# Kernel tuning notes

Hardware: AMD Instinct MI355X
Metric: run time of the kernel (lower is better)

Reference implementation:

```python
import jax, jax.numpy as jnp
import numpy as np

GAZE_DIR = -1.0  # dataset != 'eyediap'
B, V, VM, LAT = 64, 5023, 3500, 556
D_IN = 3 * 224 * 224


def _skew(v):  # [B,3] -> [B,3,3]
    z = jnp.zeros_like(v[:, 0])
    return jnp.stack([
        jnp.stack([z, -v[:, 2], v[:, 1]], axis=1),
        jnp.stack([v[:, 2], z, -v[:, 0]], axis=1),
        jnp.stack([-v[:, 1], v[:, 0], z], axis=1)], axis=1)


def _axis_angle_to_matrix(aa):  # [B,3] -> [B,3,3], Rodrigues
    theta = jnp.linalg.norm(aa, axis=1, keepdims=True)
    axis = aa / jnp.maximum(theta, 1e-8)
    K = _skew(axis)
    s = jnp.sin(theta)[:, :, None]
    c = jnp.cos(theta)[:, :, None]
    return jnp.eye(3, dtype=aa.dtype) + s * K + (1.0 - c) * (K @ K)


def _find_gaze_R(init_gaze):  # rotation taking init_gaze -> [0,0,GAZE_DIR]
    a = init_gaze[:, 0, :]
    a = a / jnp.linalg.norm(a, axis=1, keepdims=True)
    b = jnp.broadcast_to(jnp.array([0.0, 0.0, GAZE_DIR], a.dtype), a.shape)
    v = jnp.cross(a, b)
    c = jnp.sum(a * b, axis=1)
    K = _skew(v)
    return jnp.eye(3, dtype=a.dtype) + K + (K @ K) * (1.0 / (1.0 + c + 1e-8))[:, None, None]


def _apply_eyeball_rotation(eyeball, centre, rot2):
    aa = jnp.concatenate([rot2, jnp.zeros_like(rot2[:, :1])], axis=1)
    R = _axis_angle_to_matrix(aa)
    return jnp.einsum('bvl,bli->bvi', eyeball - centre, R) + centre


def _forward(x, enc_W, enc_b, v_template, shape_basis, camera_parameters,
             landmarks, masked_landmarks, face_mask, lmask, rmask):
    b = x.shape[0]
    latent = x.reshape(b, -1) @ enc_W + enc_b  # encoder stub
    shape_p = latent[:, :400]
    face_rot = latent[:, 545:548]
    face_t = latent[:, 548:551]
    face_scale = latent[:, 551:552] + 1.0
    l_rot = latent[:, 552:554]
    r_rot = latent[:, 554:556]

    # FLAME shape model stub: template + linear blendshapes
    vert = v_template[None] + jnp.einsum('bs,svc->bvc', shape_p, shape_basis)
    vmean = vert.mean(axis=1, keepdims=True)
    vert = (jnp.einsum('bvl,bli->bvi', vert - vmean, _axis_angle_to_matrix(face_rot))
            * face_scale[:, :, None] + face_t[:, None, :])

    l_eye = vert[:, lmask]
    r_eye = vert[:, rmask]
    l_c = l_eye.mean(axis=1, keepdims=True)
    r_c = r_eye.mean(axis=1, keepdims=True)
    idx4 = landmarks[jnp.array([19, 22, 25, 28])]
    idx2 = landmarks[jnp.array([14, 18])]
    face_centre = (vert[:, idx4].mean(1) + vert[:, idx2].mean(1)) / 2.0

    l_init = vert[:, None, 4051] - l_c
    l_init = l_init / jnp.linalg.norm(l_init, axis=2, keepdims=True)
    r_init = vert[:, None, 4597] - r_c
    r_init = r_init / jnp.linalg.norm(r_init, axis=2, keepdims=True)

    le = jnp.einsum('bvl,bli->bvi', l_eye - l_c, _find_gaze_R(l_init)) + l_c
    re = jnp.einsum('bvl,bli->bvi', r_eye - r_c, _find_gaze_R(r_init)) + r_c
    le = _apply_eyeball_rotation(le, l_c, l_rot)
    re = _apply_eyeball_rotation(re, r_c, r_rot)
    # masks are disjoint: vert_no_eyes + vert_eyes == scatter back rotated eyes
    vert = vert.at[:, lmask].set(le).at[:, rmask].set(re)

    gdir = jnp.broadcast_to(jnp.array([0.0, 0.0, GAZE_DIR], vert.dtype), (b, 1, 3))
    zc = jnp.zeros((b, 1, 3), vert.dtype)
    left_gaze = _apply_eyeball_rotation(gdir, zc, l_rot)
    right_gaze = _apply_eyeball_rotation(gdir, zc, r_rot)

    lr_cross = jnp.cross(right_gaze, left_gaze, axis=2)
    A = jnp.concatenate([left_gaze, -right_gaze, lr_cross], axis=1).transpose(0, 2, 1)
    rhs = (r_c - l_c).transpose(0, 2, 1)
    sol = jnp.linalg.solve(A, rhs)  # [B,3,1]
    gp_l = l_c + sol[:, 0:1, :] * left_gaze
    gp_r = r_c + sol[:, 1:2, :] * right_gaze
    gp_mid = (gp_l + gp_r) / 2.0
    dist = jnp.linalg.norm(gp_l - gp_r, axis=2)  # [B,1]

    vmk = vert[:, face_mask]
    fl3d = vmk[:, masked_landmarks]
    # renderer stub: pinhole projection with [B,3,4] camera
    homog = jnp.concatenate([vmk, jnp.ones_like(vmk[..., :1])], axis=-1)
    p = jnp.einsum('bij,bvj->bvi', camera_parameters, homog)
    z = p[..., 2:3]
    zs = jnp.where(z >= 0, 1.0, -1.0) * jnp.maximum(jnp.abs(z), 1e-3)
    vert_img = jnp.concatenate([p[..., :2] / zs, z], axis=-1)

    dist_row = jnp.repeat(dist[:, :, None], 3, axis=2)  # [B,1,3]
    out = jnp.concatenate([
        vmk, vert_img, fl3d, l_c, r_c, face_centre[:, None, :],
        gp_l, gp_r, gp_mid,
        l_c + left_gaze * 1000.0, r_c + right_gaze * 1000.0,
        left_gaze, right_gaze, dist_row], axis=1)  # [B, 2*VM+68+11, 3]
    return out


def setup_inputs() -> dict:
    key = jax.random.key(0)
    ks = jax.random.split(key, 8)
    x = jax.random.normal(ks[0], (B, 3, 224, 224), jnp.float32)
    enc_W = jax.random.normal(ks[1], (D_IN, LAT), jnp.float32) * 1e-3
    enc_b = jax.random.normal(ks[2], (LAT,), jnp.float32) * 0.1
    v_template = jax.random.normal(ks[3], (V, 3), jnp.float32)
    shape_basis = jax.random.normal(ks[4], (400, V, 3), jnp.float32) * 0.01
    camera_parameters = jax.random.normal(ks[5], (B, 3, 4), jnp.float32)
    landmarks = jax.random.randint(ks[6], (68,), 0, VM)
    masked_landmarks = jax.random.randint(ks[7], (68,), 0, VM)
    face_mask = jnp.arange(VM)
    left_eyeball_mask = jnp.arange(3931, 4477)   # contains 4051
    right_eyeball_mask = jnp.arange(4477, 5023)  # contains 4597
    return {"x": x, "enc_W": enc_W, "enc_b": enc_b, "v_template": v_template,
            "shape_basis": shape_basis, "camera_parameters": camera_parameters,
            "landmarks": landmarks, "masked_landmarks": masked_landmarks,
            "face_mask": face_mask, "left_eyeball_mask": left_eyeball_mask,
            "right_eyeball_mask": right_eyeball_mask}


def reference(x, enc_W, enc_b, v_template, shape_basis, camera_parameters,
              landmarks, masked_landmarks, face_mask, left_eyeball_mask,
              right_eyeball_mask):
    return _forward(x, enc_W, enc_b, v_template, shape_basis, camera_parameters,
                    landmarks, masked_landmarks, face_mask, left_eyeball_mask,
                    right_eyeball_mask)
```

## Files before the change

kernel.cpp:

```cpp
#include <hip/hip_runtime.h>
#include <hip/hip_bf16.h>
#include <math.h>

#define B_    64
#define V_    5023
#define VM_   3500
#define LAT_  556
#define DIN_  150528
#define NS_   400
#define N2_   15069
#define ROWS_ 7079
#define LE0_  3931
#define RE0_  4477
#define NEYE_ 546

#define WS_LATENT 0
#define WS_VERT0  35584
#define WS_VERT   1000000
#define WS_PB     1964416
#define PB_STRIDE 32

__global__ void k_init_latent(const float* __restrict__ enc_b,
                              float* __restrict__ latent) {
    int i = blockIdx.x * 256 + threadIdx.x;
    if (i < B_ * LAT_) latent[i] = enc_b[i % LAT_];
}

__global__ __launch_bounds__(256) void k_gemm(const float* __restrict__ x,
                                              const float* __restrict__ W,
                                              float* __restrict__ latent) {
    __shared__ float xs[16][64];
    __shared__ float wsm[16][64];
    const int n0  = blockIdx.x * 64;
    const int k0  = blockIdx.y * 1024;
    const int tid = threadIdx.x;
    const int tb  = tid >> 4;
    const int tn  = tid & 15;
    const int lb  = tid >> 2;
    const int lk4 = (tid & 3) << 2;
    const int wkk = tid >> 4;
    const int wn4 = (tid & 15) << 2;
    const int nb  = n0 + wn4;
    const bool wvalid = nb < LAT_;
    float acc[4][4] = {{0.f,0.f,0.f,0.f},{0.f,0.f,0.f,0.f},
                       {0.f,0.f,0.f,0.f},{0.f,0.f,0.f,0.f}};
    for (int kt = 0; kt < 1024; kt += 16) {
        const int kb = k0 + kt;
        float4 xv = *(const float4*)(x + (size_t)lb * DIN_ + kb + lk4);
        float4 wv = make_float4(0.f, 0.f, 0.f, 0.f);
        if (wvalid) wv = *(const float4*)(W + (size_t)(kb + wkk) * LAT_ + nb);
        __syncthreads();
        xs[lk4 + 0][lb] = xv.x;
        xs[lk4 + 1][lb] = xv.y;
        xs[lk4 + 2][lb] = xv.z;
        xs[lk4 + 3][lb] = xv.w;
        *(float4*)&wsm[wkk][wn4] = wv;
        __syncthreads();
#pragma unroll
        for (int kk = 0; kk < 16; ++kk) {
            float4 av = *(const float4*)&xs[kk][tb << 2];
            float4 bv = *(const float4*)&wsm[kk][tn << 2];
            float a[4] = {av.x, av.y, av.z, av.w};
            float b4[4] = {bv.x, bv.y, bv.z, bv.w};
#pragma unroll
            for (int i = 0; i < 4; ++i)
#pragma unroll
                for (int j = 0; j < 4; ++j)
                    acc[i][j] = fmaf(a[i], b4[j], acc[i][j]);
        }
    }
#pragma unroll
    for (int i = 0; i < 4; ++i) {
        int bbi = (tb << 2) + i;
#pragma unroll
        for (int j = 0; j < 4; ++j) {
            int nn = n0 + (tn << 2) + j;
            if (nn < LAT_) atomicAdd(&latent[bbi * LAT_ + nn], acc[i][j]);
        }
    }
}

__global__ __launch_bounds__(256) void k_shape(const float* __restrict__ latent,
                                               const float* __restrict__ sb,
                                               const float* __restrict__ vt,
                                               float* __restrict__ vert0) {
    __shared__ float ps[16][64];
    __shared__ float bs[16][64];
    const int n0  = blockIdx.x * 64;
    const int tid = threadIdx.x;
    const int tb  = tid >> 4;
    const int tn  = tid & 15;
    const int lb  = tid >> 2;
    const int ls4 = (tid & 3) << 2;
    const int wss = tid >> 4;
    const int wn4 = (tid & 15) << 2;
    float acc[4][4];
#pragma unroll
    for (int j = 0; j < 4; ++j) {
        int nn = n0 + (tn << 2) + j;
        float v = (nn < N2_) ? vt[nn] : 0.f;
#pragma unroll
        for (int i = 0; i < 4; ++i) acc[i][j] = v;
    }
    for (int st = 0; st < NS_; st += 16) {
        float4 pv = *(const float4*)(latent + lb * LAT_ + st + ls4);
        float wv[4];
#pragma unroll
        for (int j = 0; j < 4; ++j) {
            int nn = n0 + wn4 + j;
            wv[j] = (nn < N2_) ? sb[(size_t)(st + wss) * N2_ + nn] : 0.f;
        }
        __syncthreads();
        ps[ls4 + 0][lb] = pv.x;
        ps[ls4 + 1][lb] = pv.y;
        ps[ls4 + 2][lb] = pv.z;
        ps[ls4 + 3][lb] = pv.w;
#pragma unroll
        for (int j = 0; j < 4; ++j) bs[wss][wn4 + j] = wv[j];
        __syncthreads();
#pragma unroll
        for (int ss = 0; ss < 16; ++ss) {
            float4 av = *(const float4*)&ps[ss][tb << 2];
            float4 bv = *(const float4*)&bs[ss][tn << 2];
            float a[4] = {av.x, av.y, av.z, av.w};
            float b4[4] = {bv.x, bv.y, bv.z, bv.w};
#pragma unroll
            for (int i = 0; i < 4; ++i)
#pragma unroll
                for (int j = 0; j < 4; ++j)
                    acc[i][j] = fmaf(a[i], b4[j], acc[i][j]);
        }
    }
#pragma unroll
    for (int i = 0; i < 4; ++i) {
#pragma unroll
        for (int j = 0; j < 4; ++j) {
            int nn = n0 + (tn << 2) + j;
            if (nn < N2_) vert0[(size_t)((tb << 2) + i) * N2_ + nn] = acc[i][j];
        }
    }
}

__device__ inline void axis_angle(const float aa0, const float aa1, const float aa2,
                                  float R[9]) {
    float th  = sqrtf(aa0 * aa0 + aa1 * aa1 + aa2 * aa2);
    float inv = 1.0f / fmaxf(th, 1e-8f);
    float v0 = aa0 * inv, v1 = aa1 * inv, v2 = aa2 * inv;
    float s = sinf(th), c = cosf(th);
    float K[9] = {0.f, -v2, v1, v2, 0.f, -v0, -v1, v0, 0.f};
    float KK[9];
#pragma unroll
    for (int i = 0; i < 3; ++i)
#pragma unroll
        for (int j = 0; j < 3; ++j)
            KK[i * 3 + j] = K[i * 3 + 0] * K[0 * 3 + j] +
                            K[i * 3 + 1] * K[1 * 3 + j] +
                            K[i * 3 + 2] * K[2 * 3 + j];
    float omc = 1.0f - c;
#pragma unroll
    for (int i = 0; i < 9; ++i) R[i] = s * K[i] + omc * KK[i];
    R[0] += 1.f; R[4] += 1.f; R[8] += 1.f;
}

__global__ __launch_bounds__(256) void k_stats(const float* __restrict__ vert0,
                                               const float* __restrict__ latent,
                                               float* __restrict__ pb) {
    const int b   = blockIdx.x;
    const int tid = threadIdx.x;
    __shared__ float red[3][256];
    float s0 = 0.f, s1 = 0.f, s2 = 0.f;
    const float* row = vert0 + (size_t)b * N2_;
    for (int i = tid; i < N2_; i += 256) {
        float v = row[i];
        int c = i % 3;
        if (c == 0) s0 += v; else if (c == 1) s1 += v; else s2 += v;
    }
    red[0][tid] = s0; red[1][tid] = s1; red[2][tid] = s2;
    __syncthreads();
    for (int off = 128; off > 0; off >>= 1) {
        if (tid < off) {
            red[0][tid] += red[0][tid + off];
            red[1][tid] += red[1][tid + off];
            red[2][tid] += red[2][tid + off];
        }
        __syncthreads();
    }
    if (tid == 0) {
        float* p = pb + b * PB_STRIDE;
        p[0] = red[0][0] / (float)V_;
        p[1] = red[1][0] / (float)V_;
        p[2] = red[2][0] / (float)V_;
        const float* lat = latent + b * LAT_;
        float R[9];
        axis_angle(lat[545], lat[546], lat[547], R);
#pragma unroll
        for (int i = 0; i < 9; ++i) p[3 + i] = R[i];
        p[12] = lat[551] + 1.0f;
        p[13] = lat[548]; p[14] = lat[549]; p[15] = lat[550];
        float Rl[9], Rr[9];
        axis_angle(lat[552], lat[553], 0.f, Rl);
        axis_angle(lat[554], lat[555], 0.f, Rr);
        p[16] = -Rl[6]; p[17] = -Rl[7]; p[18] = -Rl[8];
        p[19] = -Rr[6]; p[20] = -Rr[7]; p[21] = -Rr[8];
    }
}

__global__ __launch_bounds__(256) void k_transform(const float* __restrict__ vert0,
                                                   const float* __restrict__ pb,
                                                   const float* __restrict__ cam,
                                                   float* __restrict__ vert,
                                                   float* __restrict__ out) {
    const int b = blockIdx.y;
    const int v = blockIdx.x * 256 + threadIdx.x;
    if (v >= V_) return;
    const float* p = pb + b * PB_STRIDE;
    const size_t vo = (size_t)b * N2_ + (size_t)v * 3;
    float w0 = vert0[vo + 0] - p[0];
    float w1 = vert0[vo + 1] - p[1];
    float w2 = vert0[vo + 2] - p[2];
    float sc = p[12];
    float r0 = (w0 * p[3] + w1 * p[6] + w2 * p[9])  * sc + p[13];
    float r1 = (w0 * p[4] + w1 * p[7] + w2 * p[10]) * sc + p[14];
    float r2 = (w0 * p[5] + w1 * p[8] + w2 * p[11]) * sc + p[15];
    vert[vo + 0] = r0; vert[vo + 1] = r1; vert[vo + 2] = r2;
    if (v < VM_) {
        size_t o = ((size_t)b * ROWS_ + v) * 3;
        out[o + 0] = r0; out[o + 1] = r1; out[o + 2] = r2;
        const float* cb = cam + b * 12;
        float p0 = cb[0] * r0 + cb[1] * r1 + cb[2]  * r2 + cb[3];
        float p1 = cb[4] * r0 + cb[5] * r1 + cb[6]  * r2 + cb[7];
        float p2 = cb[8] * r0 + cb[9] * r1 + cb[10] * r2 + cb[11];
        float zs = (p2 >= 0.f ? 1.f : -1.f) * fmaxf(fabsf(p2), 0.001f);
        size_t o2 = ((size_t)b * ROWS_ + VM_ + v) * 3;
        out[o2 + 0] = p0 / zs; out[o2 + 1] = p1 / zs; out[o2 + 2] = p2;
    }
}

__global__ __launch_bounds__(256) void k_final(const float* __restrict__ vert,
                                               const float* __restrict__ pb,
                                               const int* __restrict__ lmk,
                                               const int* __restrict__ mlmk,
                                               float* __restrict__ out) {
    const int b   = blockIdx.x;
    const int tid = threadIdx.x;
    __shared__ float red[6][256];
    const float* row = vert + (size_t)b * N2_;
    float l0 = 0.f, l1 = 0.f, l2 = 0.f, r0 = 0.f, r1 = 0.f, r2 = 0.f;
    for (int i = tid; i < 2 * NEYE_ * 3; i += 256) {
        float v = row[LE0_ * 3 + i];
        int c = i % 3;
        if (i < NEYE_ * 3) {
            if (c == 0) l0 += v; else if (c == 1) l1 += v; else l2 += v;
        } else {
            if (c == 0) r0 += v; else if (c == 1) r1 += v; else r2 += v;
        }
    }
    red[0][tid] = l0; red[1][tid] = l1; red[2][tid] = l2;
    red[3][tid] = r0; red[4][tid] = r1; red[5][tid] = r2;
    __syncthreads();
    for (int off = 128; off > 0; off >>= 1) {
        if (tid < off) {
#pragma unroll
            for (int q = 0; q < 6; ++q) red[q][tid] += red[q][tid + off];
        }
        __syncthreads();
    }
    if (tid < 204) {
        int j = tid / 3, c = tid % 3;
        int vi = mlmk[j];
        out[((size_t)b * ROWS_ + 7000 + j) * 3 + c] = row[(size_t)vi * 3 + c];
    }
    if (tid == 0) {
        float lc[3], rc[3];
        const float invn = 1.0f / (float)NEYE_;
#pragma unroll
        for (int c = 0; c < 3; ++c) { lc[c] = red[c][0] * invn; rc[c] = red[3 + c][0] * invn; }
        int i4a = lmk[19], i4b = lmk[22], i4c = lmk[25], i4d = lmk[28];
        int i2a = lmk[14], i2b = lmk[18];
        float fc[3];
#pragma unroll
        for (int c = 0; c < 3; ++c) {
            float m4 = (row[i4a * 3 + c] + row[i4b * 3 + c] +
                        row[i4c * 3 + c] + row[i4d * 3 + c]) * 0.25f;
            float m2 = (row[i2a * 3 + c] + row[i2b * 3 + c]) * 0.5f;
            fc[c] = (m4 + m2) * 0.5f;
        }
        const float* p = pb + b * PB_STRIDE;
        float lg[3] = {p[16], p[17], p[18]};
        float rg[3] = {p[19], p[20], p[21]};
        float cr[3] = {rg[1] * lg[2] - rg[2] * lg[1],
                       rg[2] * lg[0] - rg[0] * lg[2],
                       rg[0] * lg[1] - rg[1] * lg[0]};
        float A[3][3], rhs[3];
#pragma unroll
        for (int i = 0; i < 3; ++i) {
            A[i][0] = lg[i]; A[i][1] = -rg[i]; A[i][2] = cr[i];
            rhs[i] = rc[i] - lc[i];
        }
        for (int k = 0; k < 3; ++k) {
            int mrow = k; float mv = fabsf(A[k][k]);
            for (int i = k + 1; i < 3; ++i) {
                float av = fabsf(A[i][k]);
                if (av > mv) { mv = av; mrow = i; }
            }
            if (mrow != k) {
                for (int j = 0; j < 3; ++j) { float t = A[k][j]; A[k][j] = A[mrow][j]; A[mrow][j] = t; }
                float t = rhs[k]; rhs[k] = rhs[mrow]; rhs[mrow] = t;
            }
            float inv = 1.0f / A[k][k];
            for (int i = k + 1; i < 3; ++i) {
                float f = A[i][k] * inv;
                for (int j = k; j < 3; ++j) A[i][j] -= f * A[k][j];
                rhs[i] -= f * rhs[k];
            }
        }
        float sol2 = rhs[2] / A[2][2];
        float sol1 = (rhs[1] - A[1][2] * sol2) / A[1][1];
        float sol0 = (rhs[0] - A[0][1] * sol1 - A[0][2] * sol2) / A[0][0];
        float gpl[3], gpr[3], gpm[3];
#pragma unroll
        for (int c = 0; c < 3; ++c) {
            gpl[c] = lc[c] + sol0 * lg[c];
            gpr[c] = rc[c] + sol1 * rg[c];
            gpm[c] = (gpl[c] + gpr[c]) * 0.5f;
        }
        float d0 = gpl[0] - gpr[0], d1 = gpl[1] - gpr[1], d2 = gpl[2] - gpr[2];
        float dist = sqrtf(d0 * d0 + d1 * d1 + d2 * d2);
        float* o = out + ((size_t)b * ROWS_ + 7068) * 3;
#pragma unroll
        for (int c = 0; c < 3; ++c) {
            o[0 * 3 + c]  = lc[c];
            o[1 * 3 + c]  = rc[c];
            o[2 * 3 + c]  = fc[c];
            o[3 * 3 + c]  = gpl[c];
            o[4 * 3 + c]  = gpr[c];
            o[5 * 3 + c]  = gpm[c];
            o[6 * 3 + c]  = lc[c] + lg[c] * 1000.0f;
            o[7 * 3 + c]  = rc[c] + rg[c] * 1000.0f;
            o[8 * 3 + c]  = lg[c];
            o[9 * 3 + c]  = rg[c];
            o[10 * 3 + c] = dist;
        }
    }
}

extern "C" void kernel_launch(void* const* d_in, const int* in_sizes, int n_in,
                              void* d_out, int out_size, void* d_ws, size_t ws_size,
                              hipStream_t stream) {
    const float* x    = (const float*)d_in[0];
    const float* W    = (const float*)d_in[1];
    const float* eb   = (const float*)d_in[2];
    const float* vt   = (const float*)d_in[3];
    const float* sb   = (const float*)d_in[4];
    const float* cam  = (const float*)d_in[5];
    const int*   lmk  = (const int*)d_in[6];
    const int*   mlmk = (const int*)d_in[7];
    float* out = (float*)d_out;
    float* ws  = (float*)d_ws;
    float* latent = ws + WS_LATENT;
    float* vert0  = ws + WS_VERT0;
    float* vert   = ws + WS_VERT;
    float* pb     = ws + WS_PB;

    k_init_latent<<<139, 256, 0, stream>>>(eb, latent);
    k_gemm<<<dim3(9, 147), 256, 0, stream>>>(x, W, latent);
    k_shape<<<236, 256, 0, stream>>>(latent, sb, vt, vert0);
    k_stats<<<64, 256, 0, stream>>>(vert0, latent, pb);
    k_transform<<<dim3(20, 64), 256, 0, stream>>>(vert0, pb, cam, vert, out);
    k_final<<<64, 256, 0, stream>>>(vert, pb, lmk, mlmk, out);
}
```

Before: 668.1 us.

## Run encoder GEMM on fp16 MFMA with hi/lo split; vectorize shape-basis loads

The encoder GEMM moves from scalar fp32 FMAs to MFMA 16x16x32 f16 instructions. Each fp32 operand is split into scaled fp16 high and low parts, and three MFMA passes (hi*hi, hi*lo, lo*hi) approximate fp32 accuracy. W tiles are converted and double-buffered in shared memory while the next tile is prefetched, and x fragments are loaded straight from global memory into registers. The shape-basis GEMM also switches to float4 loads where the row is fully in range. The fixed scale factors risk fp16 overflow or underflow if input magnitudes differ from what is expected, and the split adds conversion overhead.

```diff
diff --git a/kernel.cpp b/kernel.cpp
--- a/kernel.cpp
+++ b/kernel.cpp
@@ -11,8 +11,15 @@
 #define N2_   15069
 #define ROWS_ 7079
 #define LE0_  3931
-#define RE0_  4477
 #define NEYE_ 546
+
+#define KC_   1024
+#define KS_   32
+#define NSUB_ (KC_/KS_)
+#define SDW_  18
+#define XSC_  64.0f
+#define WSC_  4096.0f
+#define OSC_  (1.0f/262144.0f)
 
 #define WS_LATENT 0
 #define WS_VERT0  35584
@@ -20,6 +27,17 @@
 #define WS_PB     1964416
 #define PB_STRIDE 32
 
+typedef _Float16 f16x8 __attribute__((ext_vector_type(8)));
+typedef float    f32x4 __attribute__((ext_vector_type(4)));
+
+union F16x8 { f16x8 v; unsigned int u[4]; _Float16 h[8]; };
+
+static __device__ inline unsigned int packh(_Float16 a, _Float16 b) {
+    union { _Float16 h; unsigned short u; } ca, cb;
+    ca.h = a; cb.h = b;
+    return (unsigned int)ca.u | ((unsigned int)cb.u << 16);
+}
+
 __global__ void k_init_latent(const float* __restrict__ enc_b,
                               float* __restrict__ latent) {
     int i = blockIdx.x * 256 + threadIdx.x;
@@ -29,55 +47,96 @@
 __global__ __launch_bounds__(256) void k_gemm(const float* __restrict__ x,
                                               const float* __restrict__ W,
                                               float* __restrict__ latent) {
-    __shared__ float xs[16][64];
-    __shared__ float wsm[16][64];
+    __shared__ __align__(16) unsigned int wt[2][2][64 * SDW_];
+    const int tid = threadIdx.x;
     const int n0  = blockIdx.x * 64;
-    const int k0  = blockIdx.y * 1024;
-    const int tid = threadIdx.x;
-    const int tb  = tid >> 4;
-    const int tn  = tid & 15;
-    const int lb  = tid >> 2;
-    const int lk4 = (tid & 3) << 2;
-    const int wkk = tid >> 4;
-    const int wn4 = (tid & 15) << 2;
-    const int nb  = n0 + wn4;
-    const bool wvalid = nb < LAT_;
-    float acc[4][4] = {{0.f,0.f,0.f,0.f},{0.f,0.f,0.f,0.f},
-                       {0.f,0.f,0.f,0.f},{0.f,0.f,0.f,0.f}};
-    for (int kt = 0; kt < 1024; kt += 16) {
-        const int kb = k0 + kt;
-        float4 xv = *(const float4*)(x + (size_t)lb * DIN_ + kb + lk4);
-        float4 wv = make_float4(0.f, 0.f, 0.f, 0.f);
-        if (wvalid) wv = *(const float4*)(W + (size_t)(kb + wkk) * LAT_ + nb);
+    const int k0  = blockIdx.y * KC_;
+    const int sq   = tid & 15;
+    const int skp  = tid >> 4;
+    const int scol = n0 + sq * 4;
+    const bool svalid = scol < LAT_;
+    const int lane = tid & 63;
+    const int w    = tid >> 6;
+    const int wr   = w >> 1;
+    const int wc   = w & 1;
+    const int c16  = lane & 15;
+    const int g    = lane >> 4;
+
+    f32x4 acc[2][2] = {};
+    float4 wv0, wv1;
+    {
+        const float* wp = W + (size_t)(k0 + 2 * skp) * LAT_ + scol;
+        wv0 = svalid ? *(const float4*)wp : make_float4(0.f, 0.f, 0.f, 0.f);
+        wv1 = svalid ? *(const float4*)(wp + LAT_) : make_float4(0.f, 0.f, 0.f, 0.f);
+    }
+    for (int s = 0; s < NSUB_; ++s) {
+        const int db = s & 1;
+        {
+            float v0[4] = {wv0.x, wv0.y, wv0.z, wv0.w};
+            float v1[4] = {wv1.x, wv1.y, wv1.z, wv1.w};
+#pragma unroll
+            for (int c = 0; c < 4; ++c) {
+                float a = v0[c] * WSC_, b = v1[c] * WSC_;
+                _Float16 h0 = (_Float16)a, h1 = (_Float16)b;
+                _Float16 l0 = (_Float16)(a - (float)h0);
+                _Float16 l1 = (_Float16)(b - (float)h1);
+                wt[db][0][(sq * 4 + c) * SDW_ + skp] = packh(h0, h1);
+                wt[db][1][(sq * 4 + c) * SDW_ + skp] = packh(l0, l1);
+            }
+        }
+        if (s + 1 < NSUB_) {
+            const float* wp = W + (size_t)(k0 + (s + 1) * KS_ + 2 * skp) * LAT_ + scol;
+            wv0 = svalid ? *(const float4*)wp : make_float4(0.f, 0.f, 0.f, 0.f);
+            wv1 = svalid ? *(const float4*)(wp + LAT_) : make_float4(0.f, 0.f, 0.f, 0.f);
+        }
         __syncthreads();
-        xs[lk4 + 0][lb] = xv.x;
-        xs[lk4 + 1][lb] = xv.y;
-        xs[lk4 + 2][lb] = xv.z;
-        xs[lk4 + 3][lb] = xv.w;
-        *(float4*)&wsm[wkk][wn4] = wv;
-        __syncthreads();
-#pragma unroll
-        for (int kk = 0; kk < 16; ++kk) {
-            float4 av = *(const float4*)&xs[kk][tb << 2];
-            float4 bv = *(const float4*)&wsm[kk][tn << 2];
-            float a[4] = {av.x, av.y, av.z, av.w};
-            float b4[4] = {bv.x, bv.y, bv.z, bv.w};
-#pragma unroll
-            for (int i = 0; i < 4; ++i)
-#pragma unroll
-                for (int j = 0; j < 4; ++j)
-                    acc[i][j] = fmaf(a[i], b4[j], acc[i][j]);
-        }
-    }
-#pragma unroll
-    for (int i = 0; i < 4; ++i) {
-        int bbi = (tb << 2) + i;
-#pragma unroll
-        for (int j = 0; j < 4; ++j) {
-            int nn = n0 + (tn << 2) + j;
-            if (nn < LAT_) atomicAdd(&latent[bbi * LAT_ + nn], acc[i][j]);
-        }
-    }
+        F16x8 ahi[2], alo[2];
+#pragma unroll
+        for (int rf = 0; rf < 2; ++rf) {
+            const int row = 32 * wr + 16 * rf + c16;
+            const float* xp = x + (size_t)row * DIN_ + k0 + s * KS_ + 8 * g;
+            float4 a0 = *(const float4*)xp;
+            float4 a1 = *(const float4*)(xp + 4);
+            float av[8] = {a0.x, a0.y, a0.z, a0.w, a1.x, a1.y, a1.z, a1.w};
+#pragma unroll
+            for (int j = 0; j < 8; ++j) {
+                float sv = av[j] * XSC_;
+                _Float16 h = (_Float16)sv;
+                ahi[rf].h[j] = h;
+                alo[rf].h[j] = (_Float16)(sv - (float)h);
+            }
+        }
+#pragma unroll
+        for (int cf = 0; cf < 2; ++cf) {
+            const int nl = 32 * wc + 16 * cf + c16;
+            const unsigned int* ph = &wt[db][0][nl * SDW_ + 4 * g];
+            const unsigned int* pl = &wt[db][1][nl * SDW_ + 4 * g];
+            F16x8 bh, bl;
+            uint2 t0 = *(const uint2*)ph;
+            uint2 t1 = *(const uint2*)(ph + 2);
+            bh.u[0] = t0.x; bh.u[1] = t0.y; bh.u[2] = t1.x; bh.u[3] = t1.y;
+            uint2 u0 = *(const uint2*)pl;
+            uint2 u1 = *(const uint2*)(pl + 2);
+            bl.u[0] = u0.x; bl.u[1] = u0.y; bl.u[2] = u1.x; bl.u[3] = u1.y;
+#pragma unroll
+            for (int rf = 0; rf < 2; ++rf) {
+                acc[rf][cf] = __builtin_amdgcn_mfma_f32_16x16x32_f16(ahi[rf].v, bh.v, acc[rf][cf], 0, 0, 0);
+                acc[rf][cf] = __builtin_amdgcn_mfma_f32_16x16x32_f16(ahi[rf].v, bl.v, acc[rf][cf], 0, 0, 0);
+                acc[rf][cf] = __builtin_amdgcn_mfma_f32_16x16x32_f16(alo[rf].v, bh.v, acc[rf][cf], 0, 0, 0);
+            }
+        }
+    }
+#pragma unroll
+    for (int rf = 0; rf < 2; ++rf)
+#pragma unroll
+        for (int cf = 0; cf < 2; ++cf)
+#pragma unroll
+            for (int i = 0; i < 4; ++i) {
+                int row = 32 * wr + 16 * rf + 4 * g + i;
+                int col = n0 + 32 * wc + 16 * cf + c16;
+                if (col < LAT_)
+                    atomicAdd(&latent[row * LAT_ + col], acc[rf][cf][i] * OSC_);
+            }
 }
 
 __global__ __launch_bounds__(256) void k_shape(const float* __restrict__ latent,
@@ -105,10 +164,16 @@
     for (int st = 0; st < NS_; st += 16) {
         float4 pv = *(const float4*)(latent + lb * LAT_ + st + ls4);
         float wv[4];
-#pragma unroll
-        for (int j = 0; j < 4; ++j) {
-            int nn = n0 + wn4 + j;
-            wv[j] = (nn < N2_) ? sb[(size_t)(st + wss) * N2_ + nn] : 0.f;
+        int nn0 = n0 + wn4;
+        if (nn0 + 3 < N2_) {
+            float4 t = *(const float4*)(sb + (size_t)(st + wss) * N2_ + nn0);
+            wv[0] = t.x; wv[1] = t.y; wv[2] = t.z; wv[3] = t.w;
+        } else {
+#pragma unroll
+            for (int j = 0; j < 4; ++j) {
+                int nn = nn0 + j;
+                wv[j] = (nn < N2_) ? sb[(size_t)(st + wss) * N2_ + nn] : 0.f;
+            }
         }
         __syncthreads();
         ps[ls4 + 0][lb] = pv.x;
```

Result: faster. 600.0 us (-10.2%).
